# Kernel tuning notes

Measured on AMD Instinct MI355X. Metric: run time of the kernel, lower is better.

The kernel has to match this reference:

```python
import jax, jax.numpy as jnp
import numpy as np

INFINITY = 1000000000000.0
HEADS = 12
HEAD_SIZE = 64


def setup_inputs() -> dict:
    key = jax.random.key(0)
    k1, k2 = jax.random.split(key)
    B, S, H = 8, 512, 1024
    x = jax.random.normal(k1, (B, S, H), dtype=jnp.float32)
    mask = jnp.ones((B, S), dtype=jnp.float32)
    W = jax.random.normal(k2, (H, HEADS * HEAD_SIZE * 2), dtype=jnp.float32) * (1.0 / np.sqrt(H))
    b = jnp.zeros((HEADS * HEAD_SIZE * 2,), dtype=jnp.float32)
    return {"x": x, "mask": mask, "W": W, "b": b}


def _sinusoidal_pos(seq_len, dim, dtype):
    # pos[n, d] interleaved as [sin0, cos0, sin1, cos1, ...]
    position = jnp.arange(seq_len, dtype=dtype)  # (S,)
    indices = jnp.power(jnp.asarray(10000.0, dtype), -2.0 * jnp.arange(dim // 2, dtype=dtype) / dim)
    ang = position[:, None] * indices[None, :]  # (S, d/2)
    pos = jnp.stack([jnp.sin(ang), jnp.cos(ang)], axis=-1).reshape(seq_len, dim)
    return pos


def reference(x, mask, W, b):
    B, S, _ = x.shape
    hs = HEAD_SIZE
    proj = x @ W + b  # (B, S, HEADS*2*hs)
    proj = proj.reshape(B, S, HEADS, 2 * hs)
    qw, kw = proj[..., :hs], proj[..., hs:]  # (B, S, HEADS, hs)

    # RoPE (note: original uses torch .repeat, i.e. TILING, not interleave)
    pos = _sinusoidal_pos(S, hs, x.dtype)  # (S, hs)
    cos_half = pos[None, :, None, 1::2]  # (1, S, 1, hs/2)
    sin_half = pos[None, :, None, ::2]
    cos_pos = jnp.concatenate([cos_half, cos_half], axis=-1)  # tiled -> (1,S,1,hs)
    sin_pos = jnp.concatenate([sin_half, sin_half], axis=-1)

    def rotate(t):
        t2 = jnp.stack([-t[..., 1::2], t[..., ::2]], axis=-1).reshape(t.shape)
        return t * cos_pos + t2 * sin_pos

    qw = rotate(qw)
    kw = rotate(kw)

    logits = jnp.einsum('bmhd,bnhd->bhmn', qw, kw)  # (B, HEADS, S, S)

    # sequence masking on dim 2 (rows) and dim 3 (cols)
    m_row = mask[:, None, :, None]
    m_col = mask[:, None, None, :]
    logits = logits * m_row + (-INFINITY) * (1.0 - m_row)
    logits = logits * m_col + (-INFINITY) * (1.0 - m_col)

    # strictly-lower-triangular mask (exclude end < start)
    tri = jnp.tril(jnp.ones((S, S), dtype=logits.dtype), k=-1)
    logits = logits - tri * INFINITY
    return logits / (hs ** 0.5)
```

## Files before the change

### kernel.cpp

```cpp
#include <hip/hip_runtime.h>
#include <stdint.h>
#include <stddef.h>

#define SS 512
#define HID 1024
#define NHEADS 12
#define HSZ 64
#define NPROJ 1536
#define NEG_INF 1000000000000.0f

typedef __attribute__((ext_vector_type(4))) float f32x4;
typedef __attribute__((ext_vector_type(8))) __bf16 bf16x8;
typedef __attribute__((ext_vector_type(4))) unsigned short us4;

typedef __attribute__((address_space(1))) unsigned char gu8;
typedef __attribute__((address_space(3))) unsigned char lu8;

static __device__ __forceinline__ void gld16(const void* g, void* l) {
  __builtin_amdgcn_global_load_lds((gu8*)(g), (lu8*)(l), 16, 0, 0);
}

static __device__ __forceinline__ unsigned short f2bf(float f) {
  union { float f; unsigned u; } x; x.f = f;
  unsigned r = x.u + 0x7fffu + ((x.u >> 16) & 1u);
  return (unsigned short)(r >> 16);
}

__global__ __launch_bounds__(256) void k_prep(
    const float4* __restrict__ x, const float* __restrict__ W,
    float2* __restrict__ tab, us4* __restrict__ xb, unsigned short* __restrict__ wbt) {
  __shared__ float t[32][33];
  const int bid = blockIdx.x;
  const int tid = threadIdx.x;
  if (bid < 64) {
    int tt = bid * 256 + tid;
    int s = tt >> 5, i = tt & 31;
    float rate = powf(10000.0f, -(float)i / 32.0f);
    float sv, cv;
    sincosf((float)s * rate, &sv, &cv);
    tab[tt] = make_float2(sv, cv);
  } else if (bid < 64 + 4096) {
    int i = (bid - 64) * 256 + tid;
    float4 v = x[i];
    us4 o;
    o[0] = f2bf(v.x); o[1] = f2bf(v.y); o[2] = f2bf(v.z); o[3] = f2bf(v.w);
    xb[i] = o;
  } else {
    int flat = bid - (64 + 4096);
    int n0 = (flat % 48) * 32, k0 = (flat / 48) * 32;
    int tx = tid & 31, ty = tid >> 5;
#pragma unroll
    for (int i = 0; i < 4; ++i)
      t[ty + i * 8][tx] = W[(k0 + ty + i * 8) * NPROJ + n0 + tx];
    __syncthreads();
#pragma unroll
    for (int i = 0; i < 4; ++i)
      wbt[(n0 + ty + i * 8) * HID + (k0 + tx)] = f2bf(t[tx][ty + i * 8]);
  }
}

__global__ __launch_bounds__(256) void k_proj(
    const unsigned short* __restrict__ xb, const unsigned short* __restrict__ wbt,
    const float* __restrict__ bias, const float2* __restrict__ tab,
    unsigned short* __restrict__ qo, unsigned short* __restrict__ ko) {
  __shared__ __align__(16) unsigned short lA[2][128 * 64];
  __shared__ __align__(16) unsigned short lB[2][96 * 64];
  const int tid = threadIdx.x;
  const int lane = tid & 63, w = tid >> 6;
  const int wm = w >> 1, wn = w & 1;
  const int m0 = blockIdx.x * 128, n0 = blockIdx.y * 96;

  const char* aptr[4]; const char* bptr[3];
  int adst[4], bdst[3];
#pragma unroll
  for (int c = 0; c < 4; ++c) {
    int lin = (w * 4 + c) * 1024 + lane * 16;
    int row = lin >> 7, cb = lin & 127;
    aptr[c] = (const char*)(xb + (size_t)(m0 + row) * HID) + (cb ^ ((row & 7) << 4));
    adst[c] = (w * 4 + c) * 1024;
  }
#pragma unroll
  for (int c = 0; c < 3; ++c) {
    int lin = (w * 3 + c) * 1024 + lane * 16;
    int row = lin >> 7, cb = lin & 127;
    bptr[c] = (const char*)(wbt + (size_t)(n0 + row) * HID) + (cb ^ ((row & 7) << 4));
    bdst[c] = (w * 3 + c) * 1024;
  }

  f32x4 acc[3][4];
#pragma unroll
  for (int a = 0; a < 3; ++a)
#pragma unroll
    for (int b = 0; b < 4; ++b)
      acc[a][b] = (f32x4)(0.0f);

#define STAGE(buf, kt)                                                      \
  do {                                                                      \
    _Pragma("unroll") for (int c = 0; c < 4; ++c)                           \
        gld16(aptr[c] + (kt) * 128, (char*)(&lA[(buf)][0]) + adst[c]);      \
    _Pragma("unroll") for (int c = 0; c < 3; ++c)                           \
        gld16(bptr[c] + (kt) * 128, (char*)(&lB[(buf)][0]) + bdst[c]);      \
  } while (0)

  STAGE(0, 0);
  asm volatile("s_waitcnt vmcnt(0)" ::: "memory");
  __builtin_amdgcn_s_barrier();

  for (int kt = 0; kt < 16; ++kt) {
    const int cur = kt & 1;
    if (kt < 15) STAGE(cur ^ 1, kt + 1);
#pragma unroll
    for (int ks = 0; ks < 2; ++ks) {
      bf16x8 af[3], bf[4];
      const int kb = ks * 64 + (lane >> 4) * 16;
#pragma unroll
      for (int a = 0; a < 3; ++a) {
        int row = wn * 48 + a * 16 + (lane & 15);
        af[a] = *(const bf16x8*)((const char*)(&lB[cur][0]) + row * 128 + (kb ^ ((row & 7) << 4)));
      }
#pragma unroll
      for (int b = 0; b < 4; ++b) {
        int row = wm * 64 + b * 16 + (lane & 15);
        bf[b] = *(const bf16x8*)((const char*)(&lA[cur][0]) + row * 128 + (kb ^ ((row & 7) << 4)));
      }
#pragma unroll
      for (int a = 0; a < 3; ++a)
#pragma unroll
        for (int b = 0; b < 4; ++b)
          acc[a][b] = __builtin_amdgcn_mfma_f32_16x16x32_bf16(af[a], bf[b], acc[a][b], 0, 0, 0);
    }
    asm volatile("s_waitcnt vmcnt(0)" ::: "memory");
    __builtin_amdgcn_s_barrier();
  }
#undef STAGE

#pragma unroll
  for (int a = 0; a < 3; ++a) {
    const int nq = n0 + wn * 48 + a * 16 + (lane >> 4) * 4;
    const float4 bv = *(const float4*)(bias + nq);
    const int d = nq & 63;
    const int h = nq >> 7;
    unsigned short* base = ((nq >> 6) & 1) ? ko : qo;
#pragma unroll
    for (int b = 0; b < 4; ++b) {
      const int mrow = m0 + wm * 64 + b * 16 + (lane & 15);
      const int s = mrow & (SS - 1);
      const int bidx = mrow >> 9;
      const float2* tp = tab + s * 32 + (d & 31);
      const float4 ta = *(const float4*)(tp);
      const float4 tb = *(const float4*)(tp + 2);
      float v0 = acc[a][b][0] + bv.x;
      float v1 = acc[a][b][1] + bv.y;
      float v2 = acc[a][b][2] + bv.z;
      float v3 = acc[a][b][3] + bv.w;
      float o0 = v0 * ta.y - v1 * ta.x;
      float o1 = v1 * ta.w + v0 * ta.z;
      float o2 = v2 * tb.y - v3 * tb.x;
      float o3 = v3 * tb.w + v2 * tb.z;
      us4 pk;
      pk[0] = f2bf(o0); pk[1] = f2bf(o1); pk[2] = f2bf(o2); pk[3] = f2bf(o3);
      *(us4*)(base + ((size_t)(bidx * NHEADS + h) * SS + s) * HSZ + d) = pk;
    }
  }
}

__global__ __launch_bounds__(256) void k_logits(
    const unsigned short* __restrict__ q, const unsigned short* __restrict__ kk,
    const float* __restrict__ mask, float* __restrict__ out) {
  const int tid = threadIdx.x;
  const int lane = tid & 63, w = tid >> 6;
  const int bh = blockIdx.y;
  const int b = bh / NHEADS;
  const int m0 = (blockIdx.x >> 2) * 128, n0 = (blockIdx.x & 3) * 128;
  const char* qbase = (const char*)(q + (size_t)bh * SS * HSZ);
  const char* kbase = (const char*)(kk + (size_t)bh * SS * HSZ);

  int mrow[4], nrow[4];
#pragma unroll
  for (int i = 0; i < 4; ++i) {
    mrow[i] = m0 + (w >> 1) * 64 + i * 16 + (lane & 15);
    nrow[i] = n0 + (w & 1) * 64 + i * 16 + (lane & 15);
  }

  f32x4 acc[4][4];
#pragma unroll
  for (int a = 0; a < 4; ++a)
#pragma unroll
    for (int bb = 0; bb < 4; ++bb)
      acc[a][bb] = (f32x4)(0.0f);

#pragma unroll
  for (int ks = 0; ks < 2; ++ks) {
    const int kboff = ks * 64 + (lane >> 4) * 16;
    bf16x8 kf[4], qf[4];
#pragma unroll
    for (int i = 0; i < 4; ++i)
      kf[i] = *(const bf16x8*)(kbase + (size_t)nrow[i] * 128 + kboff);
#pragma unroll
    for (int i = 0; i < 4; ++i)
      qf[i] = *(const bf16x8*)(qbase + (size_t)mrow[i] * 128 + kboff);
#pragma unroll
    for (int ni = 0; ni < 4; ++ni)
#pragma unroll
      for (int mi = 0; mi < 4; ++mi)
        acc[ni][mi] = __builtin_amdgcn_mfma_f32_16x16x32_bf16(kf[ni], qf[mi], acc[ni][mi], 0, 0, 0);
  }

#pragma unroll
  for (int mi = 0; mi < 4; ++mi) {
    const int m = mrow[mi];
    const float mr = mask[b * SS + m];
    float* orow = out + ((size_t)bh * SS + m) * SS;
#pragma unroll
    for (int ni = 0; ni < 4; ++ni) {
      const int nb = n0 + (w & 1) * 64 + ni * 16 + (lane >> 4) * 4;
      const float4 mc = *(const float4*)(mask + b * SS + nb);
      f32x4 res;
#pragma unroll
      for (int r = 0; r < 4; ++r) {
        float v = acc[ni][mi][r];
        const float mcv = (r == 0) ? mc.x : (r == 1) ? mc.y : (r == 2) ? mc.z : mc.w;
        v = v * mr - NEG_INF * (1.0f - mr);
        v = v * mcv - NEG_INF * (1.0f - mcv);
        if (m > nb + r) v -= NEG_INF;
        res[r] = v * 0.125f;
      }
      *(f32x4*)(orow + nb) = res;
    }
  }
}

extern "C" void kernel_launch(void* const* d_in, const int* in_sizes, int n_in,
                              void* d_out, int out_size, void* d_ws, size_t ws_size,
                              hipStream_t stream) {
  const float* x = (const float*)d_in[0];
  const float* mask = (const float*)d_in[1];
  const float* W = (const float*)d_in[2];
  const float* bias = (const float*)d_in[3];
  float* out = (float*)d_out;

  char* ws = (char*)d_ws;
  float2* tab = (float2*)ws;
  unsigned short* xb = (unsigned short*)(ws + 131072);
  unsigned short* wbt = (unsigned short*)(ws + 131072 + 8388608);
  unsigned short* qo = (unsigned short*)(ws + 131072 + 8388608 + 3145728);
  unsigned short* ko = (unsigned short*)(ws + 131072 + 8388608 + 3145728 + 6291456);

  k_prep<<<dim3(64 + 4096 + 1536), dim3(256), 0, stream>>>(
      (const float4*)x, W, tab, (us4*)xb, wbt);
  k_proj<<<dim3(32, 16), dim3(256), 0, stream>>>(xb, wbt, bias, tab, qo, ko);
  k_logits<<<dim3(16, 96), dim3(256), 0, stream>>>(qo, ko, mask, out);
}
```

Baseline: 59.44 us.

## Skip QK MFMA on fully masked tiles and single-buffer projection LDS

In the logits kernel, tiles that lie entirely below the diagonal now skip the Q/K loads and MFMAs. Those outputs are dominated by the -1e12 triangular bias, so zero accumulators should round to the same fp32 value. Separately, the projection GEMM drops its double-buffered LDS staging in favour of a single buffer with load, sync, compute, sync per k-step. This halves LDS use and may raise occupancy, but it serialises global-to-LDS loads with compute. The logits kernel is likely dominated by its large fp32 output writes, so the compute skip has limited headroom.

```diff
diff --git a/kernel.cpp b/kernel.cpp
--- a/kernel.cpp
+++ b/kernel.cpp
@@ -63,8 +63,8 @@
     const unsigned short* __restrict__ xb, const unsigned short* __restrict__ wbt,
     const float* __restrict__ bias, const float2* __restrict__ tab,
     unsigned short* __restrict__ qo, unsigned short* __restrict__ ko) {
-  __shared__ __align__(16) unsigned short lA[2][128 * 64];
-  __shared__ __align__(16) unsigned short lB[2][96 * 64];
+  __shared__ __align__(16) unsigned short lA[128 * 64];
+  __shared__ __align__(16) unsigned short lB[96 * 64];
   const int tid = threadIdx.x;
   const int lane = tid & 63, w = tid >> 6;
   const int wm = w >> 1, wn = w & 1;
@@ -94,21 +94,14 @@
     for (int b = 0; b < 4; ++b)
       acc[a][b] = (f32x4)(0.0f);
 
-#define STAGE(buf, kt)                                                      \
-  do {                                                                      \
-    _Pragma("unroll") for (int c = 0; c < 4; ++c)                           \
-        gld16(aptr[c] + (kt) * 128, (char*)(&lA[(buf)][0]) + adst[c]);      \
-    _Pragma("unroll") for (int c = 0; c < 3; ++c)                           \
-        gld16(bptr[c] + (kt) * 128, (char*)(&lB[(buf)][0]) + bdst[c]);      \
-  } while (0)
-
-  STAGE(0, 0);
-  asm volatile("s_waitcnt vmcnt(0)" ::: "memory");
-  __builtin_amdgcn_s_barrier();
-
   for (int kt = 0; kt < 16; ++kt) {
-    const int cur = kt & 1;
-    if (kt < 15) STAGE(cur ^ 1, kt + 1);
+#pragma unroll
+    for (int c = 0; c < 4; ++c)
+      gld16(aptr[c] + kt * 128, (char*)lA + adst[c]);
+#pragma unroll
+    for (int c = 0; c < 3; ++c)
+      gld16(bptr[c] + kt * 128, (char*)lB + bdst[c]);
+    __syncthreads();
 #pragma unroll
     for (int ks = 0; ks < 2; ++ks) {
       bf16x8 af[3], bf[4];
@@ -116,12 +109,12 @@
 #pragma unroll
       for (int a = 0; a < 3; ++a) {
         int row = wn * 48 + a * 16 + (lane & 15);
-        af[a] = *(const bf16x8*)((const char*)(&lB[cur][0]) + row * 128 + (kb ^ ((row & 7) << 4)));
+        af[a] = *(const bf16x8*)((const char*)lB + row * 128 + (kb ^ ((row & 7) << 4)));
       }
 #pragma unroll
       for (int b = 0; b < 4; ++b) {
         int row = wm * 64 + b * 16 + (lane & 15);
-        bf[b] = *(const bf16x8*)((const char*)(&lA[cur][0]) + row * 128 + (kb ^ ((row & 7) << 4)));
+        bf[b] = *(const bf16x8*)((const char*)lA + row * 128 + (kb ^ ((row & 7) << 4)));
       }
 #pragma unroll
       for (int a = 0; a < 3; ++a)
@@ -129,10 +122,8 @@
         for (int b = 0; b < 4; ++b)
           acc[a][b] = __builtin_amdgcn_mfma_f32_16x16x32_bf16(af[a], bf[b], acc[a][b], 0, 0, 0);
     }
-    asm volatile("s_waitcnt vmcnt(0)" ::: "memory");
-    __builtin_amdgcn_s_barrier();
-  }
-#undef STAGE
+    __syncthreads();
+  }
 
 #pragma unroll
   for (int a = 0; a < 3; ++a) {
@@ -174,6 +165,7 @@
   const int m0 = (blockIdx.x >> 2) * 128, n0 = (blockIdx.x & 3) * 128;
   const char* qbase = (const char*)(q + (size_t)bh * SS * HSZ);
   const char* kbase = (const char*)(kk + (size_t)bh * SS * HSZ);
+  const bool full_masked = (n0 + 128 <= m0);
 
   int mrow[4], nrow[4];
 #pragma unroll
@@ -189,21 +181,23 @@
     for (int bb = 0; bb < 4; ++bb)
       acc[a][bb] = (f32x4)(0.0f);
 
-#pragma unroll
-  for (int ks = 0; ks < 2; ++ks) {
-    const int kboff = ks * 64 + (lane >> 4) * 16;
-    bf16x8 kf[4], qf[4];
-#pragma unroll
-    for (int i = 0; i < 4; ++i)
-      kf[i] = *(const bf16x8*)(kbase + (size_t)nrow[i] * 128 + kboff);
-#pragma unroll
-    for (int i = 0; i < 4; ++i)
-      qf[i] = *(const bf16x8*)(qbase + (size_t)mrow[i] * 128 + kboff);
-#pragma unroll
-    for (int ni = 0; ni < 4; ++ni)
-#pragma unroll
-      for (int mi = 0; mi < 4; ++mi)
-        acc[ni][mi] = __builtin_amdgcn_mfma_f32_16x16x32_bf16(kf[ni], qf[mi], acc[ni][mi], 0, 0, 0);
+  if (!full_masked) {
+#pragma unroll
+    for (int ks = 0; ks < 2; ++ks) {
+      const int kboff = ks * 64 + (lane >> 4) * 16;
+      bf16x8 kf[4], qf[4];
+#pragma unroll
+      for (int i = 0; i < 4; ++i)
+        kf[i] = *(const bf16x8*)(kbase + (size_t)nrow[i] * 128 + kboff);
+#pragma unroll
+      for (int i = 0; i < 4; ++i)
+        qf[i] = *(const bf16x8*)(qbase + (size_t)mrow[i] * 128 + kboff);
+#pragma unroll
+      for (int ni = 0; ni < 4; ++ni)
+#pragma unroll
+        for (int mi = 0; mi < 4; ++mi)
+          acc[ni][mi] = __builtin_amdgcn_mfma_f32_16x16x32_bf16(kf[ni], qf[mi], acc[ni][mi], 0, 0, 0);
+    }
   }
 
 #pragma unroll
```

Measured after the change: 64.02 us. 7.7% more time.
